# Kernel optimization log

Hardware: AMD Instinct MI355X
Metric: run time of the kernel (lower is better)

Reference implementation:

```python
import jax, jax.numpy as jnp
import numpy as np

# Config mirrors CrossAttentionAudio2T(dim=768, n_head=12, num_frames=16, spec_frames=8,
# attn_all_frame=True, audio_patch=196, time_encoding=False, use_stpos=True)
B, T, N, NA, ST, D, H = 4, 8, 196, 196, 8, 768, 12
HD = D // H
SCALE = HD ** -0.5


def setup_inputs() -> dict:
    key = jax.random.key(0)
    ks = jax.random.split(key, 12)
    r = lambda k, s: jax.random.normal(k, s, dtype=jnp.float32)
    return dict(
        t_x=r(ks[0], (B, T * N, D)),
        audio=r(ks[1], (NA + 2, B * ST, D)),
        vmae_space_pos=SCALE * r(ks[2], (N, D)),
        audio_space_pos=SCALE * r(ks[3], (NA, D)),
        vmae_temporal_pos=SCALE * r(ks[4], (T, D)),
        audio_temporal_pos=SCALE * r(ks[5], (ST, D)),
        q_w=0.02 * r(ks[6], (D, D)),
        q_b=jnp.zeros((D,), jnp.float32),
        kv_w=0.02 * r(ks[7], (2 * D, D)),
        kv_b=jnp.zeros((2 * D,), jnp.float32),
        proj_w=0.02 * r(ks[8], (D, D)),
        proj_b=jnp.zeros((D,), jnp.float32),
    )


def reference(t_x, audio, vmae_space_pos, audio_space_pos, vmae_temporal_pos,
              audio_temporal_pos, q_w, q_b, kv_w, kv_b, proj_w, proj_b):
    # --- video query tokens: add spatial + temporal pos embeds ---
    x = t_x.reshape(B, T, N, D) + vmae_space_pos          # [B,T,N,D] + [N,D]
    x = x.transpose(0, 2, 1, 3) + vmae_temporal_pos       # [B,N,T,D] + [T,D]
    x = x.transpose(0, 2, 1, 3).reshape(B, T * N, D)      # 'b n t d -> b (t n) d'

    # --- audio key/value tokens: drop 2 lead tokens, add pos embeds ---
    a = audio[2:].reshape(NA, B, ST, D).transpose(1, 2, 0, 3)  # 'n (b t) d -> b t n d'
    a = a + audio_space_pos                                    # [B,ST,NA,D] + [NA,D]
    a = a.transpose(0, 2, 1, 3) + audio_temporal_pos           # [B,NA,ST,D] + [ST,D]
    a = a.reshape(B, NA * ST, D)                               # 'b n t d -> b (n t) d'

    # --- projections ---
    q = (x @ q_w.T + q_b).reshape(B, T * N, H, HD).transpose(0, 2, 1, 3)   # [B,H,Lq,HD]
    kv = (a @ kv_w.T + kv_b).reshape(B, NA * ST, 2, H, HD)
    k = kv[:, :, 0].transpose(0, 2, 1, 3)                                  # [B,H,Lk,HD]
    v = kv[:, :, 1].transpose(0, 2, 1, 3)

    # --- scaled dot-product cross-attention (full score matrix, as in source) ---
    attn = jax.nn.softmax(jnp.einsum('bhqd,bhkd->bhqk', q * SCALE, k), axis=-1)
    o = jnp.einsum('bhqk,bhkd->bhqd', attn, v)
    o = o.transpose(0, 2, 1, 3).reshape(B, T * N, D)
    return o @ proj_w.T + proj_b
```

## Files before the change

kernel.cpp:

```cpp
#include <hip/hip_runtime.h>

typedef short s8v __attribute__((ext_vector_type(8)));
typedef short s4v __attribute__((ext_vector_type(4)));
typedef float f4v __attribute__((ext_vector_type(4)));

#define LQ 1568
#define LK 1568
#define NH 12
#define LQP 1664

__device__ __forceinline__ unsigned short f2bf(float f) {
  union { float f; unsigned u; } x; x.f = f;
  unsigned r = x.u + 0x7FFFu + ((x.u >> 16) & 1u);
  return (unsigned short)(r >> 16);
}
__device__ __forceinline__ float bf2f(unsigned s) {
  union { unsigned u; float f; } x; x.u = s << 16;
  return x.f;
}

__global__ void prep_all(const float* __restrict__ t_x, const float* __restrict__ audio,
                         const float* __restrict__ sp, const float* __restrict__ asp,
                         const float* __restrict__ tp, const float* __restrict__ atp,
                         const float* __restrict__ q_w, const float* __restrict__ kv_w,
                         const float* __restrict__ proj_w,
                         unsigned short* __restrict__ xb, unsigned short* __restrict__ ab,
                         unsigned short* __restrict__ wq, unsigned short* __restrict__ wkv,
                         unsigned short* __restrict__ wp, int total4) {
  const int n1 = 768 * 768 / 4, n2 = 1536 * 768 / 4;
  const int nconv = 2 * n1 + n2;
  int i = blockIdx.x * 256 + threadIdx.x;
  if (i < nconv) {
    const float* src; unsigned short* dst; int j = i;
    if (i < n1)           { src = q_w;    dst = wq;  }
    else if (i < n1 + n2) { src = kv_w;   dst = wkv; j = i - n1; }
    else                  { src = proj_w; dst = wp;  j = i - n1 - n2; }
    float4 v = *(const float4*)(src + (size_t)j * 4);
    ushort4 o;
    o.x = f2bf(v.x); o.y = f2bf(v.y); o.z = f2bf(v.z); o.w = f2bf(v.w);
    *(ushort4*)(dst + (size_t)j * 4) = o;
    return;
  }
  i -= nconv;
  if (i >= 2 * total4) return;
  if (i < total4) {
    int d4 = (i % 192) * 4;
    int row = i / 192;
    int l = row % LQ;
    int t = l / 196, n = l % 196;
    float4 a  = *(const float4*)(t_x + (size_t)i * 4);
    float4 s  = *(const float4*)(sp + n * 768 + d4);
    float4 tt = *(const float4*)(tp + t * 768 + d4);
    ushort4 o;
    o.x = f2bf(a.x + s.x + tt.x);
    o.y = f2bf(a.y + s.y + tt.y);
    o.z = f2bf(a.z + s.z + tt.z);
    o.w = f2bf(a.w + s.w + tt.w);
    *(ushort4*)(xb + (size_t)i * 4) = o;
  } else {
    i -= total4;
    int d4 = (i % 192) * 4;
    int row = i / 192;
    int b = row / LK;
    int r2 = row % LK;
    int na = r2 >> 3, ta = r2 & 7;
    const float* src = audio + ((size_t)(2 + na) * 32 + b * 8 + ta) * 768 + d4;
    float4 a  = *(const float4*)src;
    float4 s  = *(const float4*)(asp + na * 768 + d4);
    float4 tt = *(const float4*)(atp + ta * 768 + d4);
    ushort4 o;
    o.x = f2bf(a.x + s.x + tt.x);
    o.y = f2bf(a.y + s.y + tt.y);
    o.z = f2bf(a.z + s.z + tt.z);
    o.w = f2bf(a.w + s.w + tt.w);
    *(ushort4*)(ab + (size_t)i * 4) = o;
  }
}

__device__ __forceinline__ void gemm_mainloop(
    const unsigned short* __restrict__ A, const unsigned short* __restrict__ W,
    int K, int row0, int col0,
    unsigned short* As, unsigned short* Bs, f4v acc[4][4]) {
  const int tid = threadIdx.x;
  const int lane = tid & 63, wave = tid >> 6;
  const int wm = wave & 1, wn = wave >> 1;
  const int l15 = lane & 15, quad = lane >> 4;
  const int lr = tid >> 3, lc = (tid & 7) * 8;

  for (int k0 = 0; k0 < K; k0 += 64) {
    __syncthreads();
#pragma unroll
    for (int it = 0; it < 4; ++it) {
      int row = lr + it * 32;
      __builtin_amdgcn_global_load_lds(
          (const __attribute__((address_space(1))) unsigned int*)(A + (size_t)(row0 + row) * K + k0 + lc),
          (__attribute__((address_space(3))) unsigned int*)(As + row * 64 + lc), 16, 0, 0);
      __builtin_amdgcn_global_load_lds(
          (const __attribute__((address_space(1))) unsigned int*)(W + (size_t)(col0 + row) * K + k0 + lc),
          (__attribute__((address_space(3))) unsigned int*)(Bs + row * 64 + lc), 16, 0, 0);
    }
    __syncthreads();
#pragma unroll
    for (int kk = 0; kk < 2; ++kk) {
      s8v af[4], bf[4];
#pragma unroll
      for (int i = 0; i < 4; ++i) {
        af[i] = *(const s8v*)(As + (wm * 64 + i * 16 + l15) * 64 + kk * 32 + quad * 8);
        bf[i] = *(const s8v*)(Bs + (wn * 64 + i * 16 + l15) * 64 + kk * 32 + quad * 8);
      }
#pragma unroll
      for (int mi = 0; mi < 4; ++mi)
#pragma unroll
        for (int ni = 0; ni < 4; ++ni)
          acc[mi][ni] = __builtin_amdgcn_mfma_f32_16x16x32_bf16(af[mi], bf[ni],
                                                               acc[mi][ni], 0, 0, 0);
    }
  }
}

__global__ __launch_bounds__(256, 4) void gemm_qkv(
    const unsigned short* __restrict__ xb, const unsigned short* __restrict__ ab,
    const unsigned short* __restrict__ wq, const unsigned short* __restrict__ wkv,
    const float* __restrict__ q_b, const float* __restrict__ kv_b,
    unsigned short* __restrict__ Qs, unsigned short* __restrict__ Kb,
    unsigned short* __restrict__ Vb) {
  __shared__ __align__(16) unsigned short As[128 * 64];
  __shared__ __align__(16) unsigned short Bs[128 * 64];
  const int tid = threadIdx.x;
  const int lane = tid & 63, wave = tid >> 6;
  const int wm = wave & 1, wn = wave >> 1;
  const int l15 = lane & 15, quad = lane >> 4;
  const int row0 = blockIdx.x * 128;
  const int y = blockIdx.y;
  const bool isQ = (y < 6);
  const int col0 = (isQ ? y : y - 6) * 128;
  const unsigned short* A = isQ ? xb : ab;
  const unsigned short* W = isQ ? wq : wkv;
  const float* bias = isQ ? q_b : kv_b;

  f4v acc[4][4] = {};
  gemm_mainloop(A, W, 768, row0, col0, As, Bs, acc);

#pragma unroll
  for (int mi = 0; mi < 4; ++mi) {
    int rowg = row0 + wm * 64 + mi * 16 + quad * 4;
#pragma unroll
    for (int ni = 0; ni < 4; ++ni) {
      int colg = col0 + wn * 64 + ni * 16 + l15;
      float bv = bias[colg];
      if (!isQ && colg >= 768) {
        int oo = colg - 768;
        int h = oo >> 6, hd = oo & 63;
        int b = rowg / LK, l0 = rowg - b * LK;
        ushort4 pk;
        pk.x = f2bf(acc[mi][ni][0] + bv);
        pk.y = f2bf(acc[mi][ni][1] + bv);
        pk.z = f2bf(acc[mi][ni][2] + bv);
        pk.w = f2bf(acc[mi][ni][3] + bv);
        *(ushort4*)(Vb + ((((size_t)b * NH + h) * 392 + (l0 >> 2)) * 64 + hd) * 4) = pk;
        continue;
      }
#pragma unroll
      for (int r = 0; r < 4; ++r) {
        float v = acc[mi][ni][r] + bv;
        int row = rowg + r;
        int b = row / LQ, l = row - b * LQ;
        int h = colg >> 6, hd = colg & 63;
        if (isQ) {
          v *= 0.18033688011112042f;
          Qs[(((size_t)b * NH + h) * LQ + l) * 64 + hd] = f2bf(v);
        } else {
          int tile = l / 112, rr = l - tile * 112;
          Kb[(((size_t)b * NH + h) * 14 + tile) * 8064 + rr * 72 + hd] = f2bf(v);
        }
      }
    }
  }
}

__global__ __launch_bounds__(256, 4) void gemm_proj(
    const unsigned short* __restrict__ A, const unsigned short* __restrict__ W,
    const float* __restrict__ bias, float* __restrict__ out) {
  __shared__ __align__(16) unsigned short As[64 * 64];
  __shared__ __align__(16) unsigned short Bs[128 * 64];
  const int tid = threadIdx.x;
  const int lane = tid & 63, wave = tid >> 6;
  const int wm = wave & 1, wn = wave >> 1;
  const int l15 = lane & 15, quad = lane >> 4;
  const int row0 = blockIdx.x * 64;
  const int col0 = blockIdx.y * 128;
  const int lr = tid >> 3, lc = (tid & 7) * 8;

  f4v acc[2][4] = {};
  for (int k0 = 0; k0 < 768; k0 += 64) {
    __syncthreads();
#pragma unroll
    for (int it = 0; it < 2; ++it) {
      int row = lr + it * 32;
      __builtin_amdgcn_global_load_lds(
          (const __attribute__((address_space(1))) unsigned int*)(A + (size_t)(row0 + row) * 768 + k0 + lc),
          (__attribute__((address_space(3))) unsigned int*)(As + row * 64 + lc), 16, 0, 0);
    }
#pragma unroll
    for (int it = 0; it < 4; ++it) {
      int row = lr + it * 32;
      __builtin_amdgcn_global_load_lds(
          (const __attribute__((address_space(1))) unsigned int*)(W + (size_t)(col0 + row) * 768 + k0 + lc),
          (__attribute__((address_space(3))) unsigned int*)(Bs + row * 64 + lc), 16, 0, 0);
    }
    __syncthreads();
#pragma unroll
    for (int kk = 0; kk < 2; ++kk) {
      s8v af[2], bf[4];
#pragma unroll
      for (int i = 0; i < 2; ++i)
        af[i] = *(const s8v*)(As + (wm * 32 + i * 16 + l15) * 64 + kk * 32 + quad * 8);
#pragma unroll
      for (int i = 0; i < 4; ++i)
        bf[i] = *(const s8v*)(Bs + (wn * 64 + i * 16 + l15) * 64 + kk * 32 + quad * 8);
#pragma unroll
      for (int mi = 0; mi < 2; ++mi)
#pragma unroll
        for (int ni = 0; ni < 4; ++ni)
          acc[mi][ni] = __builtin_amdgcn_mfma_f32_16x16x32_bf16(af[mi], bf[ni],
                                                               acc[mi][ni], 0, 0, 0);
    }
  }

#pragma unroll
  for (int mi = 0; mi < 2; ++mi) {
    int rowg = row0 + wm * 32 + mi * 16 + quad * 4;
#pragma unroll
    for (int ni = 0; ni < 4; ++ni) {
      int colg = col0 + wn * 64 + ni * 16 + l15;
      float bv = bias[colg];
#pragma unroll
      for (int r = 0; r < 4; ++r)
        out[(size_t)(rowg + r) * 768 + colg] = acc[mi][ni][r] + bv;
    }
  }
}

__global__ __launch_bounds__(256, 4) void attn(
    const unsigned short* __restrict__ Q, const unsigned short* __restrict__ Kg,
    const unsigned short* __restrict__ Vsw,
    unsigned short* __restrict__ Op, float* __restrict__ Lp, int Z) {
  __shared__ __align__(16) unsigned short Kl[112 * 72];
  __shared__ __align__(16) unsigned short Vl[112 * 64];
  const int tid = threadIdx.x;
  const int lane = tid & 63, wave = tid >> 6;
  const int l15 = lane & 15, quad = lane >> 4;
  const int bh = blockIdx.y;
  const int q0 = blockIdx.x * 128;
  const int z = blockIdx.z;
  const int t0 = (z * 14) / Z, t1 = ((z + 1) * 14) / Z;
  const size_t base = (size_t)bh * LK * 64;

  s8v qf[2][2];
#pragma unroll
  for (int mt = 0; mt < 2; ++mt)
#pragma unroll
    for (int kk = 0; kk < 2; ++kk) {
      int row = q0 + wave * 32 + mt * 16 + l15;
      if (row > LQ - 1) row = LQ - 1;
      qf[mt][kk] = *(const s8v*)(Q + base + (size_t)row * 64 + kk * 32 + quad * 8);
    }

  f4v of[2][4] = {};
  float lr[2] = {0.0f, 0.0f};

  for (int kt = t0; kt < t1; ++kt) {
    __syncthreads();
    const unsigned short* Ksrc = Kg + ((size_t)bh * 14 + kt) * 8064;
    for (int c = tid; c < 1008; c += 256)
      __builtin_amdgcn_global_load_lds(
          (const __attribute__((address_space(1))) unsigned int*)(Ksrc + c * 8),
          (__attribute__((address_space(3))) unsigned int*)(Kl + c * 8), 16, 0, 0);
    const unsigned short* Vsrc = Vsw + base + (size_t)kt * 112 * 64;
    for (int c = tid; c < 896; c += 256)
      __builtin_amdgcn_global_load_lds(
          (const __attribute__((address_space(1))) unsigned int*)(Vsrc + c * 8),
          (__attribute__((address_space(3))) unsigned int*)(Vl + c * 8), 16, 0, 0);
    __syncthreads();

#pragma unroll
    for (int nt = 0; nt < 7; ++nt) {
      s8v kf0 = *(const s8v*)(Kl + (nt * 16 + l15) * 72 + quad * 8);
      s8v kf1 = *(const s8v*)(Kl + (nt * 16 + l15) * 72 + 32 + quad * 8);
      s4v pf[2];
#pragma unroll
      for (int mt = 0; mt < 2; ++mt) {
        f4v s = {};
        s = __builtin_amdgcn_mfma_f32_16x16x32_bf16(kf0, qf[mt][0], s, 0, 0, 0);
        s = __builtin_amdgcn_mfma_f32_16x16x32_bf16(kf1, qf[mt][1], s, 0, 0, 0);
        float p0 = __builtin_amdgcn_exp2f(s[0]);
        float p1 = __builtin_amdgcn_exp2f(s[1]);
        float p2 = __builtin_amdgcn_exp2f(s[2]);
        float p3 = __builtin_amdgcn_exp2f(s[3]);
        lr[mt] += (p0 + p1) + (p2 + p3);
        union { float f; unsigned u; } a0, a1, a2, a3;
        a0.f = p0; a1.f = p1; a2.f = p2; a3.f = p3;
        union { uint2 u; s4v s; } pk;
        pk.u.x = __builtin_amdgcn_perm(a1.u, a0.u, 0x07060302u);
        pk.u.y = __builtin_amdgcn_perm(a3.u, a2.u, 0x07060302u);
        pf[mt] = pk.s;
      }
#pragma unroll
      for (int nd = 0; nd < 4; ++nd) {
        s4v vf = *(const s4v*)(Vl + ((nt * 4 + quad) << 8) + ((nd * 16 + l15) << 2));
        of[0][nd] = __builtin_amdgcn_mfma_f32_16x16x16bf16_1k(pf[0], vf, of[0][nd], 0, 0, 0);
        of[1][nd] = __builtin_amdgcn_mfma_f32_16x16x16bf16_1k(pf[1], vf, of[1][nd], 0, 0, 0);
      }
    }
  }

#pragma unroll
  for (int mt = 0; mt < 2; ++mt) {
    lr[mt] += __shfl_xor(lr[mt], 16);
    lr[mt] += __shfl_xor(lr[mt], 32);
  }

  const size_t bbase = (((size_t)z * 48 + bh) * 13 + blockIdx.x) * 8192;
#pragma unroll
  for (int mt = 0; mt < 2; ++mt) {
#pragma unroll
    for (int nd = 0; nd < 4; ++nd) {
      union { uint2 u; ushort4 s; } pk;
      pk.s.x = f2bf(of[mt][nd][0]);
      pk.s.y = f2bf(of[mt][nd][1]);
      pk.s.z = f2bf(of[mt][nd][2]);
      pk.s.w = f2bf(of[mt][nd][3]);
      *(uint2*)(Op + bbase + (size_t)(((wave * 2 + mt) * 4 + nd) * 256 + lane * 4)) = pk.u;
    }
    if (quad == 0)
      Lp[((size_t)z * 48 + bh) * LQP + q0 + wave * 32 + mt * 16 + l15] = lr[mt];
  }
}

__global__ void attn_merge(const unsigned short* __restrict__ Op,
                           const float* __restrict__ Lp,
                           unsigned short* __restrict__ Om, int Z) {
  int i = blockIdx.x * 256 + threadIdx.x;
  int c = i & 2047;
  int t = i >> 11;
  int x = t % 13, bh = t / 13;
  int lane = c & 63, fo = c >> 6;
  int nd = fo & 3, wm = fo >> 2;
  int quad = lane >> 4, l15 = lane & 15;
  int rowl = (wm >> 1) * 32 + (wm & 1) * 16 + quad * 4;
  int col = nd * 16 + l15;
  float acc[4] = {};
  float ls[4] = {};
  for (int z = 0; z < Z; ++z) {
    size_t zb = (size_t)z * 48 + bh;
    uint2 v = *(const uint2*)(Op + (zb * 13 + x) * 8192 + (size_t)c * 4);
    acc[0] += bf2f(v.x & 0xffffu); acc[1] += bf2f(v.x >> 16);
    acc[2] += bf2f(v.y & 0xffffu); acc[3] += bf2f(v.y >> 16);
    float4 lv = *(const float4*)(Lp + zb * LQP + x * 128 + rowl);
    ls[0] += lv.x; ls[1] += lv.y; ls[2] += lv.z; ls[3] += lv.w;
  }
  int b = bh / NH, h = bh - b * NH;
#pragma unroll
  for (int r = 0; r < 4; ++r) {
    int l = x * 128 + rowl + r;
    if (l >= LQ) continue;
    Om[((size_t)b * LQ + l) * 768 + h * 64 + col] = f2bf(acc[r] / ls[r]);
  }
}

extern "C" void kernel_launch(void* const* d_in, const int* in_sizes, int n_in,
                              void* d_out, int out_size, void* d_ws, size_t ws_size,
                              hipStream_t stream) {
  const float* t_x    = (const float*)d_in[0];
  const float* audio  = (const float*)d_in[1];
  const float* sp     = (const float*)d_in[2];
  const float* asp    = (const float*)d_in[3];
  const float* tp     = (const float*)d_in[4];
  const float* atp    = (const float*)d_in[5];
  const float* q_w    = (const float*)d_in[6];
  const float* q_b    = (const float*)d_in[7];
  const float* kv_w   = (const float*)d_in[8];
  const float* kv_b   = (const float*)d_in[9];
  const float* proj_w = (const float*)d_in[10];
  const float* proj_b = (const float*)d_in[11];
  float* out = (float*)d_out;

  char* ws = (char*)d_ws;
  size_t off = 0;
  auto alloc = [&](size_t bytes) -> void* {
    void* p = ws + off;
    off += (bytes + 255) & ~(size_t)255;
    return p;
  };
  const size_t TOK = 6272;
  unsigned short* xb  = (unsigned short*)alloc(TOK * 768 * 2);
  unsigned short* ab  = (unsigned short*)alloc(TOK * 768 * 2);
  unsigned short* wq  = (unsigned short*)alloc(768 * 768 * 2);
  unsigned short* wkv = (unsigned short*)alloc(1536 * 768 * 2);
  unsigned short* wp  = (unsigned short*)alloc(768 * 768 * 2);
  unsigned short* Qs  = (unsigned short*)alloc(TOK * 768 * 2);
  unsigned short* Kb  = (unsigned short*)alloc((size_t)48 * 14 * 8064 * 2);
  unsigned short* Vb  = (unsigned short*)alloc(TOK * 768 * 2);

  auto need = [&](int Zq) {
    return off + (size_t)Zq * 48 * 13 * 8192 * 2 + (size_t)Zq * 48 * LQP * 4 + 512;
  };
  int Z;
  unsigned short* Op;
  float* Lp;
  if (ws_size >= need(4)) {
    Z = 4;
    Op = (unsigned short*)alloc((size_t)4 * 48 * 13 * 8192 * 2);
    Lp = (float*)alloc((size_t)4 * 48 * LQP * 4);
  } else {
    Z = 2;
    Op = (unsigned short*)ws;
    Lp = (float*)(ws + (size_t)2 * 48 * 13 * 8192 * 2);
  }
  unsigned short* Om = Qs;

  dim3 blk(256);
  const int n1 = 768 * 768 / 4, n2 = 1536 * 768 / 4;
  int total4 = (int)(TOK * 192);
  int nprep = 2 * n1 + n2 + 2 * total4;
  prep_all<<<dim3((nprep + 255) / 256), blk, 0, stream>>>(
      t_x, audio, sp, asp, tp, atp, q_w, kv_w, proj_w, xb, ab, wq, wkv, wp, total4);

  gemm_qkv<<<dim3(49, 18), blk, 0, stream>>>(xb, ab, wq, wkv, q_b, kv_b, Qs, Kb, Vb);

  attn<<<dim3(13, 48, Z), blk, 0, stream>>>(Qs, Kb, Vb, Op, Lp, Z);

  attn_merge<<<dim3(48 * 13 * 2048 / 256), blk, 0, stream>>>(Op, Lp, Om, Z);

  gemm_proj<<<dim3(98, 6), blk, 0, stream>>>(Om, wp, proj_b, out);
}
```

Measured before the change: 229.1 us.

## Fuse split-K attention merge into attn via atomic counters; stage QKV epilogue through LDS

New measurement: 610.4 us. +166.5%, slower.

```diff
diff --git a/kernel.cpp b/kernel.cpp
--- a/kernel.cpp
+++ b/kernel.cpp
@@ -26,7 +26,7 @@
                          const float* __restrict__ proj_w,
                          unsigned short* __restrict__ xb, unsigned short* __restrict__ ab,
                          unsigned short* __restrict__ wq, unsigned short* __restrict__ wkv,
-                         unsigned short* __restrict__ wp, int total4) {
+                         unsigned short* __restrict__ wp, int* cnt, int total4) {
   const int n1 = 768 * 768 / 4, n2 = 1536 * 768 / 4;
   const int nconv = 2 * n1 + n2;
   int i = blockIdx.x * 256 + threadIdx.x;
@@ -42,7 +42,11 @@
     return;
   }
   i -= nconv;
-  if (i >= 2 * total4) return;
+  if (i >= 2 * total4) {
+    int iz = i - 2 * total4;
+    if (cnt && iz < 624) cnt[iz] = 0;
+    return;
+  }
   if (i < total4) {
     int d4 = (i % 192) * 4;
     int row = i / 192;
@@ -77,59 +81,20 @@
   }
 }
 
-__device__ __forceinline__ void gemm_mainloop(
-    const unsigned short* __restrict__ A, const unsigned short* __restrict__ W,
-    int K, int row0, int col0,
-    unsigned short* As, unsigned short* Bs, f4v acc[4][4]) {
-  const int tid = threadIdx.x;
-  const int lane = tid & 63, wave = tid >> 6;
-  const int wm = wave & 1, wn = wave >> 1;
-  const int l15 = lane & 15, quad = lane >> 4;
-  const int lr = tid >> 3, lc = (tid & 7) * 8;
-
-  for (int k0 = 0; k0 < K; k0 += 64) {
-    __syncthreads();
-#pragma unroll
-    for (int it = 0; it < 4; ++it) {
-      int row = lr + it * 32;
-      __builtin_amdgcn_global_load_lds(
-          (const __attribute__((address_space(1))) unsigned int*)(A + (size_t)(row0 + row) * K + k0 + lc),
-          (__attribute__((address_space(3))) unsigned int*)(As + row * 64 + lc), 16, 0, 0);
-      __builtin_amdgcn_global_load_lds(
-          (const __attribute__((address_space(1))) unsigned int*)(W + (size_t)(col0 + row) * K + k0 + lc),
-          (__attribute__((address_space(3))) unsigned int*)(Bs + row * 64 + lc), 16, 0, 0);
-    }
-    __syncthreads();
-#pragma unroll
-    for (int kk = 0; kk < 2; ++kk) {
-      s8v af[4], bf[4];
-#pragma unroll
-      for (int i = 0; i < 4; ++i) {
-        af[i] = *(const s8v*)(As + (wm * 64 + i * 16 + l15) * 64 + kk * 32 + quad * 8);
-        bf[i] = *(const s8v*)(Bs + (wn * 64 + i * 16 + l15) * 64 + kk * 32 + quad * 8);
-      }
-#pragma unroll
-      for (int mi = 0; mi < 4; ++mi)
-#pragma unroll
-        for (int ni = 0; ni < 4; ++ni)
-          acc[mi][ni] = __builtin_amdgcn_mfma_f32_16x16x32_bf16(af[mi], bf[ni],
-                                                               acc[mi][ni], 0, 0, 0);
-    }
-  }
-}
-
 __global__ __launch_bounds__(256, 4) void gemm_qkv(
     const unsigned short* __restrict__ xb, const unsigned short* __restrict__ ab,
     const unsigned short* __restrict__ wq, const unsigned short* __restrict__ wkv,
     const float* __restrict__ q_b, const float* __restrict__ kv_b,
     unsigned short* __restrict__ Qs, unsigned short* __restrict__ Kb,
     unsigned short* __restrict__ Vb) {
-  __shared__ __align__(16) unsigned short As[128 * 64];
-  __shared__ __align__(16) unsigned short Bs[128 * 64];
+  __shared__ __align__(16) unsigned short sm[128 * 136];
+  unsigned short* As = sm;
+  unsigned short* Bs = sm + 8192;
   const int tid = threadIdx.x;
   const int lane = tid & 63, wave = tid >> 6;
   const int wm = wave & 1, wn = wave >> 1;
   const int l15 = lane & 15, quad = lane >> 4;
+  const int lr = tid >> 3, lc = (tid & 7) * 8;
   const int row0 = blockIdx.x * 128;
   const int y = blockIdx.y;
   const bool isQ = (y < 6);
@@ -139,16 +104,44 @@
   const float* bias = isQ ? q_b : kv_b;
 
   f4v acc[4][4] = {};
-  gemm_mainloop(A, W, 768, row0, col0, As, Bs, acc);
-
-#pragma unroll
-  for (int mi = 0; mi < 4; ++mi) {
-    int rowg = row0 + wm * 64 + mi * 16 + quad * 4;
-#pragma unroll
-    for (int ni = 0; ni < 4; ++ni) {
-      int colg = col0 + wn * 64 + ni * 16 + l15;
-      float bv = bias[colg];
-      if (!isQ && colg >= 768) {
+  for (int k0 = 0; k0 < 768; k0 += 64) {
+    __syncthreads();
+#pragma unroll
+    for (int it = 0; it < 4; ++it) {
+      int row = lr + it * 32;
+      __builtin_amdgcn_global_load_lds(
+          (const __attribute__((address_space(1))) unsigned int*)(A + (size_t)(row0 + row) * 768 + k0 + lc),
+          (__attribute__((address_space(3))) unsigned int*)(As + row * 64 + lc), 16, 0, 0);
+      __builtin_amdgcn_global_load_lds(
+          (const __attribute__((address_space(1))) unsigned int*)(W + (size_t)(col0 + row) * 768 + k0 + lc),
+          (__attribute__((address_space(3))) unsigned int*)(Bs + row * 64 + lc), 16, 0, 0);
+    }
+    __syncthreads();
+#pragma unroll
+    for (int kk = 0; kk < 2; ++kk) {
+      s8v af[4], bf[4];
+#pragma unroll
+      for (int i = 0; i < 4; ++i) {
+        af[i] = *(const s8v*)(As + (wm * 64 + i * 16 + l15) * 64 + kk * 32 + quad * 8);
+        bf[i] = *(const s8v*)(Bs + (wn * 64 + i * 16 + l15) * 64 + kk * 32 + quad * 8);
+      }
+#pragma unroll
+      for (int mi = 0; mi < 4; ++mi)
+#pragma unroll
+        for (int ni = 0; ni < 4; ++ni)
+          acc[mi][ni] = __builtin_amdgcn_mfma_f32_16x16x32_bf16(af[mi], bf[ni],
+                                                               acc[mi][ni], 0, 0, 0);
+    }
+  }
+
+  if (!isQ && col0 >= 768) {
+#pragma unroll
+    for (int mi = 0; mi < 4; ++mi) {
+      int rowg = row0 + wm * 64 + mi * 16 + quad * 4;
+#pragma unroll
+      for (int ni = 0; ni < 4; ++ni) {
+        int colg = col0 + wn * 64 + ni * 16 + l15;
+        float bv = bias[colg];
         int oo = colg - 768;
         int h = oo >> 6, hd = oo & 63;
         int b = rowg / LK, l0 = rowg - b * LK;
@@ -158,23 +151,42 @@
         pk.z = f2bf(acc[mi][ni][2] + bv);
         pk.w = f2bf(acc[mi][ni][3] + bv);
         *(ushort4*)(Vb + ((((size_t)b * NH + h) * 392 + (l0 >> 2)) * 64 + hd) * 4) = pk;
-        continue;
       }
-#pragma unroll
-      for (int r = 0; r < 4; ++r) {
-        float v = acc[mi][ni][r] + bv;
-        int row = rowg + r;
-        int b = row / LQ, l = row - b * LQ;
-        int h = colg >> 6, hd = colg & 63;
-        if (isQ) {
-          v *= 0.18033688011112042f;
-          Qs[(((size_t)b * NH + h) * LQ + l) * 64 + hd] = f2bf(v);
-        } else {
-          int tile = l / 112, rr = l - tile * 112;
-          Kb[(((size_t)b * NH + h) * 14 + tile) * 8064 + rr * 72 + hd] = f2bf(v);
-        }
-      }
-    }
+    }
+    return;
+  }
+
+  const float sc = isQ ? 0.18033688011112042f : 1.0f;
+  __syncthreads();
+#pragma unroll
+  for (int mi = 0; mi < 4; ++mi) {
+    int rl = wm * 64 + mi * 16 + quad * 4;
+#pragma unroll
+    for (int ni = 0; ni < 4; ++ni) {
+      int cl = wn * 64 + ni * 16 + l15;
+      float bv = bias[col0 + cl];
+#pragma unroll
+      for (int r = 0; r < 4; ++r)
+        sm[(rl + r) * 136 + cl] = f2bf((acc[mi][ni][r] + bv) * sc);
+    }
+  }
+  __syncthreads();
+  {
+    int row = tid >> 1, half = tid & 1;
+    int gl = row0 + row;
+    int b = gl / LQ, l = gl - b * LQ;
+    const unsigned short* src = sm + row * 136 + half * 64;
+    unsigned short* dst;
+    if (isQ) {
+      dst = Qs + (((size_t)b * NH + (col0 >> 6) + half) * LQ + l) * 64;
+    } else {
+      int h = (col0 >> 6) + half;
+      int tile = l / 112, rr = l - tile * 112;
+      dst = Kb + (((size_t)b * NH + h) * 14 + tile) * 8064 + rr * 72;
+    }
+#pragma unroll
+    for (int j = 0; j < 8; ++j)
+      *(uint4*)(dst + j * 8) = *(const uint4*)(src + j * 8);
   }
 }
 
@@ -244,9 +256,11 @@
 __global__ __launch_bounds__(256, 4) void attn(
     const unsigned short* __restrict__ Q, const unsigned short* __restrict__ Kg,
     const unsigned short* __restrict__ Vsw,
-    unsigned short* __restrict__ Op, float* __restrict__ Lp, int Z) {
+    unsigned short* __restrict__ Op, float* __restrict__ Lp,
+    unsigned short* __restrict__ Om, int* cnt, int Z) {
   __shared__ __align__(16) unsigned short Kl[112 * 72];
   __shared__ __align__(16) unsigned short Vl[112 * 64];
+  __shared__ int do_merge_s;
   const int tid = threadIdx.x;
   const int lane = tid & 63, wave = tid >> 6;
   const int l15 = lane & 15, quad = lane >> 4;
@@ -334,6 +348,40 @@
     }
     if (quad == 0)
       Lp[((size_t)z * 48 + bh) * LQP + q0 + wave * 32 + mt * 16 + l15] = lr[mt];
+  }
+
+  if (!cnt) return;
+
+  __threadfence();
+  if (tid == 0)
+    do_merge_s = (atomicAdd(&cnt[blockIdx.x * 48 + bh], 1) == Z - 1);
+  __syncthreads();
+  if (!do_merge_s) return;
+  __threadfence();
+
+  const int b = bh / NH, h = bh - b * NH;
+#pragma unroll
+  for (int k = 0; k < 8; ++k) {
+    int c = tid + k * 256;
+    int fo = c >> 6, lc2 = c & 63;
+    int nd = fo & 3, wmm = fo >> 2;
+    int rowl = (wmm >> 1) * 32 + (wmm & 1) * 16 + ((lc2 >> 4) << 2);
+    int col = nd * 16 + (lc2 & 15);
+    float a0 = 0, a1 = 0, a2 = 0, a3 = 0, s0 = 0, s1 = 0, s2 = 0, s3 = 0;
+    for (int zz = 0; zz < Z; ++zz) {
+      size_t zb = (size_t)zz * 48 + bh;
+      uint2 v = *(const uint2*)(Op + (zb * 13 + blockIdx.x) * 8192 + (size_t)c * 4);
+      a0 += bf2f(v.x & 0xffffu); a1 += bf2f(v.x >> 16);
+      a2 += bf2f(v.y & 0xffffu); a3 += bf2f(v.y >> 16);
+      float4 lv = *(const float4*)(Lp + zb * LQP + q0 + rowl);
+      s0 += lv.x; s1 += lv.y; s2 += lv.z; s3 += lv.w;
+    }
+    int l0 = q0 + rowl;
+    unsigned short* dst = Om + ((size_t)b * LQ + l0) * 768 + h * 64 + col;
+    if (l0 + 0 < LQ) dst[0]        = f2bf(a0 / s0);
+    if (l0 + 1 < LQ) dst[768]      = f2bf(a1 / s1);
+    if (l0 + 2 < LQ) dst[2 * 768]  = f2bf(a2 / s2);
+    if (l0 + 3 < LQ) dst[3 * 768]  = f2bf(a3 / s3);
   }
 }
 
@@ -405,32 +453,41 @@
   auto need = [&](int Zq) {
     return off + (size_t)Zq * 48 * 13 * 8192 * 2 + (size_t)Zq * 48 * LQP * 4 + 512;
   };
-  int Z;
-  unsigned short* Op;
+  int Z, fused;
+  unsigned short *Op, *Om;
   float* Lp;
-  if (ws_size >= need(4)) {
-    Z = 4;
+  int* cnt = nullptr;
+  if (ws_size >= need(4) + 8192) {
+    Z = 4; fused = 1;
     Op = (unsigned short*)alloc((size_t)4 * 48 * 13 * 8192 * 2);
     Lp = (float*)alloc((size_t)4 * 48 * LQP * 4);
+    cnt = (int*)alloc(624 * 4);
+    Om = xb;
+  } else if (ws_size >= need(4)) {
+    Z = 4; fused = 0;
+    Op = (unsigned short*)alloc((size_t)4 * 48 * 13 * 8192 * 2);
+    Lp = (float*)alloc((size_t)4 * 48 * LQP * 4);
+    Om = Qs;
   } else {
-    Z = 2;
+    Z = 2; fused = 0;
     Op = (unsigned short*)ws;
     Lp = (float*)(ws + (size_t)2 * 48 * 13 * 8192 * 2);
-  }
-  unsigned short* Om = Qs;
+    Om = Qs;
+  }
 
   dim3 blk(256);
   const int n1 = 768 * 768 / 4, n2 = 1536 * 768 / 4;
   int total4 = (int)(TOK * 192);
-  int nprep = 2 * n1 + n2 + 2 * total4;
+  int nprep = 2 * n1 + n2 + 2 * total4 + 624;
   prep_all<<<dim3((nprep + 255) / 256), blk, 0, stream>>>(
-      t_x, audio, sp, asp, tp, atp, q_w, kv_w, proj_w, xb, ab, wq, wkv, wp, total4);
+      t_x, audio, sp, asp, tp, atp, q_w, kv_w, proj_w, xb, ab, wq, wkv, wp, cnt, total4);
 
   gemm_qkv<<<dim3(49, 18), blk, 0, stream>>>(xb, ab, wq, wkv, q_b, kv_b, Qs, Kb, Vb);
 
-  attn<<<dim3(13, 48, Z), blk, 0, stream>>>(Qs, Kb, Vb, Op, Lp, Z);
-
-  attn_merge<<<dim3(48 * 13 * 2048 / 256), blk, 0, stream>>>(Op, Lp, Om, Z);
+  attn<<<dim3(13, 48, Z), blk, 0, stream>>>(Qs, Kb, Vb, Op, Lp, Om, cnt, Z);
+
+  if (!fused)
+    attn_merge<<<dim3(48 * 13 * 2048 / 256), blk, 0, stream>>>(Op, Lp, Om, Z);
 
   gemm_proj<<<dim3(98, 6), blk, 0, stream>>>(Om, wp, proj_b, out);
 }
```
